# Performance work log

Measured on AMD Instinct MI355X. Metric: run time of the kernel, lower is better.

The kernel has to match this reference:

```python
import jax, jax.numpy as jnp
import numpy as np

CL = 128   # context_length
IL = 64    # inst_length
PC = 256; CH1 = 256; CH2 = 256; CH3 = 256
CK1 = 3; CK2 = 3; CK3 = 3
F1 = 512; OUT = 1
F1_INPUT = CH3 * (CL - 1 - CK1 - CK2 - CK3 + 3)  # 256*121 = 30976
B = 2048


def _conv1d(x, w, b):
    # x: [B, Cin, L], w: [Cout, Cin, K] -> [B, Cout, L-K+1]
    y = jax.lax.conv_general_dilated(x, w, window_strides=(1,), padding='VALID',
                                     dimension_numbers=('NCH', 'OIH', 'NCH'))
    return y + b[None, :, None]


def setup_inputs() -> dict:
    key = jax.random.key(0)
    ks = jax.random.split(key, 13)
    def w(k, shape, fan_in):
        bound = 1.0 / np.sqrt(fan_in)
        return jax.random.uniform(k, shape, jnp.float32, -bound, bound)
    return {
        'x':   jax.random.normal(ks[0], (B, CL * IL), jnp.float32),
        'Wp':  w(ks[1], (PC, IL, 2), IL * 2),
        'bp':  w(ks[2], (PC,), IL * 2),
        'W1':  w(ks[3], (CH1, PC, CK1), PC * CK1),
        'b1':  w(ks[4], (CH1,), PC * CK1),
        'W2':  w(ks[5], (CH2, CH1, CK2), CH1 * CK2),
        'b2':  w(ks[6], (CH2,), CH1 * CK2),
        'W3':  w(ks[7], (CH3, CH2, CK3), CH2 * CK3),
        'b3':  w(ks[8], (CH3,), CH2 * CK3),
        'Wf1': w(ks[9], (F1, F1_INPUT), F1_INPUT),
        'bf1': w(ks[10], (F1,), F1_INPUT),
        'Wf2': w(ks[11], (OUT, F1), F1),
        'bf2': w(ks[12], (OUT,), F1),
    }


def reference(x, Wp, bp, W1, b1, W2, b2, W3, b3, Wf1, bf1, Wf2, bf2):
    # [B, CL*IL] -> [B, IL, CL]
    xt = x.reshape(-1, CL, IL).transpose(0, 2, 1)
    # Fused pairwise convp: the torch loop computes, for i in 1..CL-1,
    #   y[:, c, i-1] = sum_j Wp[c,j,0]*x[:,j,0] + Wp[c,j,1]*x[:,j,i] + bp[c]
    x0 = xt[:, :, 0]          # [B, IL]
    xr = xt[:, :, 1:]         # [B, IL, CL-1]
    y = (jnp.einsum('bj,cj->bc', x0, Wp[:, :, 0])[:, :, None]
         + jnp.einsum('bjl,cj->bcl', xr, Wp[:, :, 1])
         + bp[None, :, None])                       # [B, PC, CL-1]
    h = jax.nn.relu(y)
    h = jax.nn.relu(_conv1d(h, W1, b1))
    h = jax.nn.relu(_conv1d(h, W2, b2))
    h = jax.nn.relu(_conv1d(h, W3, b3))
    h = h.reshape(-1, F1_INPUT)
    h = jax.nn.relu(h @ Wf1.T + bf1)
    return h @ Wf2.T + bf2    # [B, OUT]
```

## Files before the change

kernel.cpp:

```cpp
#include <hip/hip_runtime.h>

typedef _Float16 f16;
typedef _Float16 f16x8 __attribute__((ext_vector_type(8)));
typedef _Float16 f16x4 __attribute__((ext_vector_type(4)));
typedef float    f32x4 __attribute__((ext_vector_type(4)));

#define B_SZ   2048
#define NCH    256
#define L0_    127
#define L1_    125
#define L2_    123
#define L3_    121
#define F1_    512
#define FCK    30976
#define KCH    968
#define SPLIT  22
#define KPS    44
#define NS_FC  22

__device__ __forceinline__ void gl16(const f16* g, f16* l) {
    __builtin_amdgcn_global_load_lds(
        (const __attribute__((address_space(1))) void*)g,
        (__attribute__((address_space(3))) void*)l, 16, 0, 0);
}

__global__ __launch_bounds__(256) void prep_w(const float* __restrict__ Wp,
                                              const float* __restrict__ W1,
                                              const float* __restrict__ W2,
                                              const float* __restrict__ W3,
                                              f16* __restrict__ wpw,
                                              f16* __restrict__ wct1,
                                              f16* __restrict__ wct2,
                                              f16* __restrict__ wct3) {
    int g = blockIdx.x;
    if (g < 128) {
        int idx = g * 256 + threadIdx.x;
        int ck = idx >> 13, co = (idx >> 5) & 255, w5 = idx & 31;
        int j = ck * 32 + w5;
        float v = (j < 64) ? Wp[co * 128 + j * 2 + 1]
                           : Wp[co * 128 + (j - 64) * 2];
        wpw[idx] = (f16)v;
        return;
    }
    int g2 = g - 128;
    const float* W = (g2 < 768) ? W1 : (g2 < 1536) ? W2 : W3;
    f16* dst = (g2 < 768) ? wct1 : (g2 < 1536) ? wct2 : wct3;
    int idx = (g2 % 768) * 256 + threadIdx.x;
    int ck = idx >> 13, co = (idx >> 5) & 255, w5 = idx & 31;
    int kt = ck * 32 + w5;
    int k = kt >> 8, ci = kt & 255;
    dst[idx] = (f16)W[((size_t)co * NCH + ci) * 3 + k];
}

__global__ __launch_bounds__(256) void prep_wf1k(const float* __restrict__ Wf1,
                                                 f16* __restrict__ wf1h) {
    __shared__ f16 t[NCH * 122];
    const int f = blockIdx.x, tid = threadIdx.x;
    const float* src = Wf1 + (size_t)f * FCK;
    for (int idx = tid; idx < FCK; idx += 256) {
        int co = idx / 121, l = idx - co * 121;
        t[co * 122 + l] = (f16)src[idx];
    }
    __syncthreads();
    f16* dst = wf1h + (size_t)f * FCK;
    for (int idx = tid; idx < FCK; idx += 256) {
        int l = idx >> 8, co = idx & 255;
        dst[idx] = t[co * 122 + l];
    }
}

#define STAGEC(WT, KS, BUF)                                                   \
  { const f16* s0_ = (WT) + (size_t)(KS) * 8192;                              \
    _Pragma("unroll")                                                         \
    for (int j = 0; j < 4; ++j) {                                             \
      int u_ = j * 256 + tid;                                                 \
      int r_ = u_ >> 2, c_ = u_ & 3, cs_ = c_ ^ ((r_ >> 2) & 3);              \
      gl16(s0_ + r_ * 32 + cs_ * 8,                                           \
           wlds + (BUF) * 8192 + (size_t)(j * 256 + w * 64) * 8); } }

#define READF(FA, FB, KS, CSTEPS)                                             \
  { const int kn_ = (KS) / (CSTEPS), cb_ = ((KS) % (CSTEPS)) * 4;             \
    const int rb_ = (KS) % 3;                                                 \
    _Pragma("unroll")                                                         \
    for (int m = 0; m < 8; ++m) {                                             \
      const int r_ = 16 * m + lr + kn_;                                       \
      FA[m] = *(const f16x8*)(ins + r_ * 256                                  \
                              + (((cb_ + lh) ^ (r_ & 7)) << 3)); }            \
    _Pragma("unroll")                                                         \
    for (int n = 0; n < 4; ++n) {                                             \
      const int co_ = wc0 + 16 * n + lr;                                      \
      FB[n] = *(const f16x8*)(wlds + rb_ * 8192                               \
                + (co_ * 4 + (lh ^ ((co_ >> 2) & 3))) * 8); } }

#define MFMA32(FA, FB)                                                        \
  __builtin_amdgcn_s_setprio(1);                                              \
  _Pragma("unroll")                                                           \
  for (int n = 0; n < 4; ++n)                                                 \
    _Pragma("unroll")                                                         \
    for (int m = 0; m < 8; ++m)                                               \
      acc[m][n] = __builtin_amdgcn_mfma_f32_16x16x32_f16(FA[m], FB[n],        \
                                                         acc[m][n], 0, 0, 0); \
  __builtin_amdgcn_s_setprio(0);

#define BODY(FCa, FCb, FNa, FNb, S, WT, CSTEPS)                               \
  STAGEC(WT, (S) + 2, ((S) + 2) % 3)                                          \
  __builtin_amdgcn_sched_barrier(0);                                          \
  asm volatile("s_waitcnt vmcnt(4) lgkmcnt(0)" ::: "memory");                 \
  __builtin_amdgcn_sched_barrier(0);                                          \
  __builtin_amdgcn_s_barrier();                                               \
  __builtin_amdgcn_sched_barrier(0);                                          \
  READF(FNa, FNb, (S) + 1, CSTEPS)                                            \
  __builtin_amdgcn_sched_barrier(0);                                          \
  MFMA32(FCa, FCb)                                                            \
  __builtin_amdgcn_sched_barrier(0);

#define LAYER_LOOP(WT, NS, CSTEPS)                                            \
  _Pragma("unroll")                                                           \
  for (int m = 0; m < 8; ++m)                                                 \
    _Pragma("unroll")                                                         \
    for (int n = 0; n < 4; ++n) acc[m][n] = (f32x4){0.f, 0.f, 0.f, 0.f};      \
  _Pragma("unroll 1")                                                         \
  for (int s = 0; s < (NS) - 2; s += 2) {                                     \
    BODY(aC, bC, aN, bN, s, WT, CSTEPS)                                       \
    BODY(aN, bN, aC, bC, s + 1, WT, CSTEPS)                                   \
  }                                                                           \
                          \
  asm volatile("s_waitcnt vmcnt(0) lgkmcnt(0)" ::: "memory");                 \
  __builtin_amdgcn_sched_barrier(0);                                          \
  __builtin_amdgcn_s_barrier();                                               \
  __builtin_amdgcn_sched_barrier(0);                                          \
  READF(aN, bN, (NS) - 1, CSTEPS)                                             \
  __builtin_amdgcn_sched_barrier(0);                                          \
  MFMA32(aC, bC)                                                              \
  __builtin_amdgcn_sched_barrier(0);                                          \
             \
  MFMA32(aN, bN)                                                              \
  __builtin_amdgcn_sched_barrier(0);

#define EPI_LDS(BIAS, LOUT)                                                   \
  {                                                                           \
    _Pragma("unroll")                                                         \
    for (int n = 0; n < 4; ++n) {                                             \
      const int co = wc0 + 16 * n + lr;                                       \
      const float e = (BIAS)[co];                                             \
      const int sl = co >> 3, el = co & 7;                                    \
      _Pragma("unroll")                                                       \
      for (int m = 0; m < 8; ++m)                                             \
        _Pragma("unroll")                                                     \
        for (int r = 0; r < 4; ++r) {                                         \
          const int l = 16 * m + lh * 4 + r;                                  \
          if (l < (LOUT)) {                                                   \
            float v = fmaxf(acc[m][n][r] + e, 0.f);                           \
            ins[l * 256 + (((sl) ^ (l & 7)) << 3) + el] = (f16)v;             \
          }                                                                   \
        }                                                                     \
    }                                                                         \
  }

#define BOUNDARY(BIAS, LOUT, NEXTWT)                                          \
  STAGEC(NEXTWT, 0, 0)                                                        \
  STAGEC(NEXTWT, 1, 1)                                                        \
  __builtin_amdgcn_sched_barrier(0);                                          \
  __builtin_amdgcn_s_barrier();                                               \
  __builtin_amdgcn_sched_barrier(0);                                          \
  EPI_LDS(BIAS, LOUT)                                                         \
  __builtin_amdgcn_sched_barrier(0);                                          \
  asm volatile("s_waitcnt vmcnt(0) lgkmcnt(0)" ::: "memory");                 \
  __builtin_amdgcn_sched_barrier(0);                                          \
  __builtin_amdgcn_s_barrier();                                               \
  __builtin_amdgcn_sched_barrier(0);                                          \
  READF(aC, bC, 0, 8)

__global__ __launch_bounds__(256, 1) void fused_conv(
        const float* __restrict__ xin,
        const f16* __restrict__ wpw,  const float* __restrict__ bp,
        const f16* __restrict__ wct1, const float* __restrict__ b1,
        const f16* __restrict__ wct2, const float* __restrict__ b2,
        const f16* __restrict__ wct3, const float* __restrict__ b3,
        f16* __restrict__ h3out) {
    __shared__ f16 ins[130 * 256];
    __shared__ f16 wlds[3 * 8192];

    const int b    = blockIdx.x;
    const int tid  = threadIdx.x;
    const int lane = tid & 63, w = tid >> 6;
    const int wc0  = w * 64;
    const int lr   = lane & 15, lh = lane >> 4;

    f32x4 acc[8][4];
    f16x8 aC[8], bC[4], aN[8], bN[4];

    STAGEC(wpw, 0, 0)
    STAGEC(wpw, 1, 1)
    {
        const float* xr = xin + (size_t)b * 8192;
        for (int u = tid; u < 130 * 16; u += 256) {
            int r = u >> 4, sl = u & 15;
            int off = (sl < 8)
                ? ((r + 1 < 128 ? (r + 1) * 64 : 127 * 64) + sl * 8)
                : (sl - 8) * 8;
            float4 v0 = *(const float4*)(xr + off);
            float4 v1 = *(const float4*)(xr + off + 4);
            f16x8 h = { (f16)v0.x, (f16)v0.y, (f16)v0.z, (f16)v0.w,
                        (f16)v1.x, (f16)v1.y, (f16)v1.z, (f16)v1.w };
            *(f16x8*)(ins + r * 256 + ((sl ^ (r & 7)) << 3)) = h;
        }
    }
    __syncthreads();
    READF(aC, bC, 0, 4)

    LAYER_LOOP(wpw, 4, 4)
    BOUNDARY(bp, L0_, wct1)

    LAYER_LOOP(wct1, 24, 8)
    BOUNDARY(b1, L1_, wct2)

    LAYER_LOOP(wct2, 24, 8)
    BOUNDARY(b2, L2_, wct3)

    LAYER_LOOP(wct3, 24, 8)
    {
        f16* ob = h3out + (size_t)b * L3_ * NCH;
#pragma unroll
        for (int n = 0; n < 4; ++n) {
            const int co = wc0 + 16 * n + lr;
            const float e = b3[co];
#pragma unroll
            for (int m = 0; m < 8; ++m)
#pragma unroll
                for (int r = 0; r < 4; ++r) {
                    const int l = 16 * m + lh * 4 + r;
                    if (l < L3_) {
                        float v = fmaxf(acc[m][n][r] + e, 0.f);
                        ob[(size_t)l * NCH + co] = (f16)v;
                    }
                }
        }
    }
}

__global__ __launch_bounds__(512, 1) void fc1k(const f16* __restrict__ A,
                                               const f16* __restrict__ Bw,
                                               float* __restrict__ part,
                                               int CB) {
    __shared__ f16 Asl[2 * 8192];
    __shared__ f16 Bsl[2 * 16384];
    const int m0 = blockIdx.x * 128, n0 = blockIdx.y * 256, sp = blockIdx.z;
    const int tid  = threadIdx.x;
    const int lane = tid & 63, w = tid >> 6;
    const int wb0  = (w >> 2) * 64, wf0 = (w & 3) * 64;
    const int lr   = lane & 15, lh = lane >> 4;
    const int ck0  = sp * KPS;

    auto stage = [&](int s2, int buf) {
        const int k0 = (ck0 + 2 * s2) * 32;
#pragma unroll
        for (int j = 0; j < 2; ++j) {
            int u = j * 512 + tid;
            int row = u >> 3, cu = u & 7;
            int cs = cu ^ (row & 7);
            gl16(A + (size_t)(m0 + row) * FCK + k0 + cs * 8,
                 Asl + buf * 8192 + (size_t)(j * 512 + w * 64) * 8);
        }
#pragma unroll
        for (int j = 0; j < 4; ++j) {
            int u = j * 512 + tid;
            int row = u >> 3, cu = u & 7;
            int cs = cu ^ (row & 7);
            gl16(Bw + (size_t)(n0 + row) * FCK + k0 + cs * 8,
                 Bsl + buf * 16384 + (size_t)(j * 512 + w * 64) * 8);
        }
    };

    f32x4 acc[4][4];
#pragma unroll
    for (int m = 0; m < 4; ++m)
#pragma unroll
        for (int n = 0; n < 4; ++n) acc[m][n] = (f32x4){0.f, 0.f, 0.f, 0.f};

    stage(0, 0);
    __syncthreads();

#pragma unroll 1
    for (int s = 0; s < NS_FC; ++s) {
        const int cur = s & 1;
        if (s + 1 < NS_FC) stage(s + 1, cur ^ 1);
        __builtin_amdgcn_sched_barrier(0);
#pragma unroll
        for (int kk = 0; kk < 2; ++kk) {
            f16x8 a[4], bf[4];
#pragma unroll
            for (int m = 0; m < 4; ++m) {
                const int row = wb0 + 16 * m + lr;
                const int un = (kk * 4 + lh) ^ (row & 7);
                a[m] = *(const f16x8*)(Asl + cur * 8192 + row * 64 + un * 8);
            }
#pragma unroll
            for (int n = 0; n < 4; ++n) {
                const int row = wf0 + 16 * n + lr;
                const int un = (kk * 4 + lh) ^ (row & 7);
                bf[n] = *(const f16x8*)(Bsl + cur * 16384 + row * 64 + un * 8);
            }
            __builtin_amdgcn_s_setprio(1);
#pragma unroll
            for (int m = 0; m < 4; ++m)
#pragma unroll
                for (int n = 0; n < 4; ++n)
                    acc[m][n] = __builtin_amdgcn_mfma_f32_16x16x32_f16(
                        a[m], bf[n], acc[m][n], 0, 0, 0);
            __builtin_amdgcn_s_setprio(0);
        }
        __builtin_amdgcn_sched_barrier(0);
        asm volatile("s_waitcnt vmcnt(0)" ::: "memory");
        __builtin_amdgcn_sched_barrier(0);
        __builtin_amdgcn_s_barrier();
    }

#pragma unroll
    for (int m = 0; m < 4; ++m)
#pragma unroll
        for (int n = 0; n < 4; ++n)
#pragma unroll
            for (int r = 0; r < 4; ++r) {
                const int bl = m0 + wb0 + 16 * m + lh * 4 + r;
                const int f  = n0 + wf0 + 16 * n + lr;
                part[((size_t)sp * CB + bl) * F1_ + f] = acc[m][n][r];
            }
}

__global__ __launch_bounds__(512) void fcout(const float* __restrict__ part,
                                             const float* __restrict__ bf1,
                                             const float* __restrict__ Wf2,
                                             const float* __restrict__ bf2,
                                             float* __restrict__ out,
                                             int CB) {
    __shared__ float red[8];
    const int m = blockIdx.x;
    const int f = threadIdx.x;
    float s = bf1[f];
#pragma unroll
    for (int sp = 0; sp < SPLIT; ++sp)
        s += part[((size_t)sp * CB + m) * F1_ + f];
    float p = fmaxf(s, 0.f) * Wf2[f];
#pragma unroll
    for (int o = 32; o > 0; o >>= 1) p += __shfl_xor(p, o);
    if ((f & 63) == 0) red[f >> 6] = p;
    __syncthreads();
    if (f < 8) {
        float v = red[f];
        v += __shfl_xor(v, 1);
        v += __shfl_xor(v, 2);
        v += __shfl_xor(v, 4);
        if (f == 0) out[m] = v + bf2[0];
    }
}

extern "C" void kernel_launch(void* const* d_in, const int* in_sizes, int n_in,
                              void* d_out, int out_size, void* d_ws, size_t ws_size,
                              hipStream_t stream) {
    const float* x   = (const float*)d_in[0];
    const float* Wp  = (const float*)d_in[1];
    const float* bp  = (const float*)d_in[2];
    const float* W1  = (const float*)d_in[3];
    const float* b1  = (const float*)d_in[4];
    const float* W2  = (const float*)d_in[5];
    const float* b2  = (const float*)d_in[6];
    const float* W3  = (const float*)d_in[7];
    const float* b3  = (const float*)d_in[8];
    const float* Wf1 = (const float*)d_in[9];
    const float* bf1 = (const float*)d_in[10];
    const float* Wf2 = (const float*)d_in[11];
    const float* bf2 = (const float*)d_in[12];
    float* out = (float*)d_out;

    char* base = (char*)d_ws;
    size_t off = 0;
    auto alloc = [&](size_t bytes) {
        size_t o = off; off = (off + bytes + 255) & ~(size_t)255; return o;
    };
    const size_t o_wpw  = alloc((size_t)NCH * 128 * 2);
    const size_t o_wct1 = alloc((size_t)NCH * 768 * 2);
    const size_t o_wct2 = alloc((size_t)NCH * 768 * 2);
    const size_t o_wct3 = alloc((size_t)NCH * 768 * 2);
    const size_t o_wf1h = alloc((size_t)F1_ * FCK * 2);
    const size_t fixed  = off;

    int CB = 0;
    const int cand[5] = {2048, 1024, 512, 256, 128};
    for (int i = 0; i < 5; ++i) {
        size_t c = (size_t)cand[i];
        size_t need = fixed
            + (((size_t)SPLIT * c * F1_ * 4 + 255) & ~(size_t)255)
            + ((c * (size_t)L3_ * NCH * 2 + 255) & ~(size_t)255);
        if (need <= ws_size) { CB = cand[i]; break; }
    }
    if (CB == 0) return;
    const int nchunk = B_SZ / CB;

    const size_t o_part = alloc((size_t)SPLIT * CB * F1_ * 4);
    const size_t o_h3   = alloc((size_t)CB * L3_ * NCH * 2);

    f16*   wpw  = (f16*)(base + o_wpw);
    f16*   wct1 = (f16*)(base + o_wct1);
    f16*   wct2 = (f16*)(base + o_wct2);
    f16*   wct3 = (f16*)(base + o_wct3);
    f16*   wf1h = (f16*)(base + o_wf1h);
    float* part = (float*)(base + o_part);
    f16*   h3   = (f16*)(base + o_h3);

    prep_w<<<2432, 256, 0, stream>>>(Wp, W1, W2, W3, wpw, wct1, wct2, wct3);
    prep_wf1k<<<F1_, 256, 0, stream>>>(Wf1, wf1h);

    for (int c = 0; c < nchunk; ++c) {
        const size_t b0 = (size_t)c * CB;
        fused_conv<<<CB, 256, 0, stream>>>(x + b0 * 8192,
                                           wpw, bp, wct1, b1, wct2, b2,
                                           wct3, b3, h3);
        fc1k<<<dim3(CB / 128, 2, SPLIT), 512, 0, stream>>>(h3, wf1h, part, CB);
        fcout<<<CB, 512, 0, stream>>>(part, bf1, Wf2, bf2, out + b0, CB);
    }
}
```

Baseline: 665.4 us.

## Single-buffer conv weights to fit two blocks per CU

Replaces the triple-buffered weight staging and register-level fragment double buffering with one weight LDS buffer and a simple load, barrier, MFMA, wait loop. The input LDS tile also shrinks to 128 rows, and launch bounds change to two blocks per CU. The aim is to cut LDS and register use so a second block can run on each CU and hide memory latency across blocks. In exchange, each block loses its own overlap of weight loads with MFMA work. Fragment reads for rows 128-129 now fall past the end of the input tile, although those rows only feed masked outputs.

```diff
diff --git a/kernel.cpp b/kernel.cpp
--- a/kernel.cpp
+++ b/kernel.cpp
@@ -69,18 +69,17 @@
     }
 }
 
-#define STAGEC(WT, KS, BUF)                                                   \
+#define STAGEC(WT, KS)                                                        \
   { const f16* s0_ = (WT) + (size_t)(KS) * 8192;                              \
     _Pragma("unroll")                                                         \
     for (int j = 0; j < 4; ++j) {                                             \
       int u_ = j * 256 + tid;                                                 \
       int r_ = u_ >> 2, c_ = u_ & 3, cs_ = c_ ^ ((r_ >> 2) & 3);              \
       gl16(s0_ + r_ * 32 + cs_ * 8,                                           \
-           wlds + (BUF) * 8192 + (size_t)(j * 256 + w * 64) * 8); } }
+           wlds + (size_t)(j * 256 + w * 64) * 8); } }
 
 #define READF(FA, FB, KS, CSTEPS)                                             \
   { const int kn_ = (KS) / (CSTEPS), cb_ = ((KS) % (CSTEPS)) * 4;             \
-    const int rb_ = (KS) % 3;                                                 \
     _Pragma("unroll")                                                         \
     for (int m = 0; m < 8; ++m) {                                             \
       const int r_ = 16 * m + lr + kn_;                                       \
@@ -89,7 +88,7 @@
     _Pragma("unroll")                                                         \
     for (int n = 0; n < 4; ++n) {                                             \
       const int co_ = wc0 + 16 * n + lr;                                      \
-      FB[n] = *(const f16x8*)(wlds + rb_ * 8192                               \
+      FB[n] = *(const f16x8*)(wlds                                            \
                 + (co_ * 4 + (lh ^ ((co_ >> 2) & 3))) * 8); } }
 
 #define MFMA32(FA, FB)                                                        \
@@ -102,40 +101,27 @@
                                                          acc[m][n], 0, 0, 0); \
   __builtin_amdgcn_s_setprio(0);
 
-#define BODY(FCa, FCb, FNa, FNb, S, WT, CSTEPS)                               \
-  STAGEC(WT, (S) + 2, ((S) + 2) % 3)                                          \
-  __builtin_amdgcn_sched_barrier(0);                                          \
-  asm volatile("s_waitcnt vmcnt(4) lgkmcnt(0)" ::: "memory");                 \
-  __builtin_amdgcn_sched_barrier(0);                                          \
-  __builtin_amdgcn_s_barrier();                                               \
-  __builtin_amdgcn_sched_barrier(0);                                          \
-  READF(FNa, FNb, (S) + 1, CSTEPS)                                            \
-  __builtin_amdgcn_sched_barrier(0);                                          \
-  MFMA32(FCa, FCb)                                                            \
-  __builtin_amdgcn_sched_barrier(0);
-
 #define LAYER_LOOP(WT, NS, CSTEPS)                                            \
   _Pragma("unroll")                                                           \
   for (int m = 0; m < 8; ++m)                                                 \
     _Pragma("unroll")                                                         \
     for (int n = 0; n < 4; ++n) acc[m][n] = (f32x4){0.f, 0.f, 0.f, 0.f};      \
   _Pragma("unroll 1")                                                         \
-  for (int s = 0; s < (NS) - 2; s += 2) {                                     \
-    BODY(aC, bC, aN, bN, s, WT, CSTEPS)                                       \
-    BODY(aN, bN, aC, bC, s + 1, WT, CSTEPS)                                   \
-  }                                                                           \
-                          \
-  asm volatile("s_waitcnt vmcnt(0) lgkmcnt(0)" ::: "memory");                 \
-  __builtin_amdgcn_sched_barrier(0);                                          \
-  __builtin_amdgcn_s_barrier();                                               \
-  __builtin_amdgcn_sched_barrier(0);                                          \
-  READF(aN, bN, (NS) - 1, CSTEPS)                                             \
-  __builtin_amdgcn_sched_barrier(0);                                          \
-  MFMA32(aC, bC)                                                              \
-  __builtin_amdgcn_sched_barrier(0);                                          \
-             \
-  MFMA32(aN, bN)                                                              \
-  __builtin_amdgcn_sched_barrier(0);
+  for (int s = 0; s < (NS); ++s) {                                            \
+    READF(aC, bC, s, CSTEPS)                                                  \
+    __builtin_amdgcn_sched_barrier(0);                                        \
+    asm volatile("s_waitcnt lgkmcnt(0)" ::: "memory");                        \
+    __builtin_amdgcn_sched_barrier(0);                                        \
+    __builtin_amdgcn_s_barrier();                                             \
+    __builtin_amdgcn_sched_barrier(0);                                        \
+    if (s + 1 < (NS)) STAGEC(WT, s + 1)                                       \
+    __builtin_amdgcn_sched_barrier(0);                                        \
+    MFMA32(aC, bC)                                                            \
+    __builtin_amdgcn_sched_barrier(0);                                        \
+    asm volatile("s_waitcnt vmcnt(0)" ::: "memory");                          \
+    __builtin_amdgcn_s_barrier();                                             \
+    __builtin_amdgcn_sched_barrier(0);                                        \
+  }
 
 #define EPI_LDS(BIAS, LOUT)                                                   \
   {                                                                           \
@@ -158,28 +144,23 @@
   }
 
 #define BOUNDARY(BIAS, LOUT, NEXTWT)                                          \
-  STAGEC(NEXTWT, 0, 0)                                                        \
-  STAGEC(NEXTWT, 1, 1)                                                        \
-  __builtin_amdgcn_sched_barrier(0);                                          \
-  __builtin_amdgcn_s_barrier();                                               \
+  STAGEC(NEXTWT, 0)                                                           \
   __builtin_amdgcn_sched_barrier(0);                                          \
   EPI_LDS(BIAS, LOUT)                                                         \
   __builtin_amdgcn_sched_barrier(0);                                          \
   asm volatile("s_waitcnt vmcnt(0) lgkmcnt(0)" ::: "memory");                 \
-  __builtin_amdgcn_sched_barrier(0);                                          \
   __builtin_amdgcn_s_barrier();                                               \
-  __builtin_amdgcn_sched_barrier(0);                                          \
-  READF(aC, bC, 0, 8)
-
-__global__ __launch_bounds__(256, 1) void fused_conv(
+  __builtin_amdgcn_sched_barrier(0);
+
+__global__ __launch_bounds__(256, 2) void fused_conv(
         const float* __restrict__ xin,
         const f16* __restrict__ wpw,  const float* __restrict__ bp,
         const f16* __restrict__ wct1, const float* __restrict__ b1,
         const f16* __restrict__ wct2, const float* __restrict__ b2,
         const f16* __restrict__ wct3, const float* __restrict__ b3,
         f16* __restrict__ h3out) {
-    __shared__ f16 ins[130 * 256];
-    __shared__ f16 wlds[3 * 8192];
+    __shared__ f16 ins[128 * 256];
+    __shared__ f16 wlds[8192];
 
     const int b    = blockIdx.x;
     const int tid  = threadIdx.x;
@@ -188,13 +169,12 @@
     const int lr   = lane & 15, lh = lane >> 4;
 
     f32x4 acc[8][4];
-    f16x8 aC[8], bC[4], aN[8], bN[4];
-
-    STAGEC(wpw, 0, 0)
-    STAGEC(wpw, 1, 1)
+    f16x8 aC[8], bC[4];
+
+    STAGEC(wpw, 0)
     {
         const float* xr = xin + (size_t)b * 8192;
-        for (int u = tid; u < 130 * 16; u += 256) {
+        for (int u = tid; u < 128 * 16; u += 256) {
             int r = u >> 4, sl = u & 15;
             int off = (sl < 8)
                 ? ((r + 1 < 128 ? (r + 1) * 64 : 127 * 64) + sl * 8)
@@ -207,7 +187,6 @@
         }
     }
     __syncthreads();
-    READF(aC, bC, 0, 4)
 
     LAYER_LOOP(wpw, 4, 4)
     BOUNDARY(bp, L0_, wct1)
```

Measured after the change: 692.5 us. 1.04x slower.
